# Kernel tuning notes

Measured on AMD Instinct MI355X. Metric: run time of the kernel, lower is better.

The kernel has to match this reference:

```python
import jax, jax.numpy as jnp
import numpy as np

M, A, H, T = 6, 4096, 128, 30   # num_modes, num_actors, hidden_size, future_steps
HIST = 50
MAX_T = 6.0
DT = MAX_T / T                   # min_stepsize: one Euler step per prediction interval
MIN_SCALE = 0.001
EPS = 1e-5

def _ln(x, g, b):
    mu = x.mean(-1, keepdims=True)
    v = ((x - mu) ** 2).mean(-1, keepdims=True)
    return (x - mu) * jax.lax.rsqrt(v + EPS) * g + b

def setup_inputs() -> dict:
    key = jax.random.key(0)
    ks = iter(jax.random.split(key, 64))
    def p(shape):
        return jax.random.normal(next(ks), shape, jnp.float32) * 0.02
    inp = {
        'local_embed':  jax.random.normal(next(ks), (A, H), jnp.float32),
        'global_embed': jax.random.normal(next(ks), (M, A, H), jnp.float32),
        'noise':        jax.random.normal(next(ks), (T, M * A, H), jnp.float32),
        # aggr_embed: Linear(2H,H) + LayerNorm
        'aggr_w': p((2 * H, H)), 'aggr_b': p((H,)),
        'aggr_g': jnp.ones((H,), jnp.float32), 'aggr_be': jnp.zeros((H,), jnp.float32),
        # FFunc (posterior drift): Linear(H+2,H)-Tanh-Linear(H,H)-Tanh-Linear(H,H)
        'f_w1': p((H + 2, H)), 'f_b1': p((H,)),
        'f_w2': p((H, H)),     'f_b2': p((H,)),
        'f_w3': p((H, H)),     'f_b3': p((H,)),
        # GFunc (diffusion): Linear(H+2,H)-Tanh-Linear(H,H)-Tanh-Linear(H,1)-Sigmoid
        'g_w1': p((H + 2, H)), 'g_b1': p((H,)),
        'g_w2': p((H, H)),     'g_b2': p((H,)),
        'g_w3': p((H, 1)),     'g_b3': p((1,)),
        # decoder: Linear(H,H)+LN+ReLU+Linear(H,2)
        'd_w1': p((H, H)), 'd_b1': p((H,)),
        'd_g': jnp.ones((H,), jnp.float32), 'd_be': jnp.zeros((H,), jnp.float32),
        'd_w2': p((H, 2)), 'd_b2': p((2,)),
        # scale head (uncertain=True): same structure as decoder
        's_w1': p((H, H)), 's_b1': p((H,)),
        's_g': jnp.ones((H,), jnp.float32), 's_be': jnp.zeros((H,), jnp.float32),
        's_w2': p((H, 2)), 's_b2': p((2,)),
        # pi head: Linear(2H,H)+LN+ReLU+Linear(H,1)
        'p_w1': p((2 * H, H)), 'p_b1': p((H,)),
        'p_g': jnp.ones((H,), jnp.float32), 'p_be': jnp.zeros((H,), jnp.float32),
        'p_w2': p((H, 1)), 'p_b2': p((1,)),
        'padding_mask': jnp.zeros((A, HIST), dtype=bool),
    }
    return inp

def reference(local_embed, global_embed, noise,
              aggr_w, aggr_b, aggr_g, aggr_be,
              f_w1, f_b1, f_w2, f_b2, f_w3, f_b3,
              g_w1, g_b1, g_w2, g_b2, g_w3, g_b3,
              d_w1, d_b1, d_g, d_be, d_w2, d_b2,
              s_w1, s_b1, s_g, s_be, s_w2, s_b2,
              p_w1, p_b1, p_g, p_be, p_w2, p_b2,
              padding_mask):
    N = M * A
    le = jnp.broadcast_to(local_embed, (M, A, H))
    # aggr_embed(cat(global, local))
    x = jnp.concatenate([global_embed, le], axis=-1)
    h0 = jax.nn.relu(_ln(x @ aggr_w + aggr_b, aggr_g, aggr_be)).reshape(N, H)

    def with_time(y, t):
        tc = jnp.ones((y.shape[0], 1), y.dtype) * t
        return jnp.concatenate([y, jnp.sin(tc), jnp.cos(tc)], axis=-1)

    def drift(t, y):  # FFunc
        i = with_time(y, t)
        h = jnp.tanh(i @ f_w1 + f_b1)
        h = jnp.tanh(h @ f_w2 + f_b2)
        return h @ f_w3 + f_b3

    def diffusion(t, y):  # GFunc -> scalar per sample, repeated over dims
        i = with_time(y, t)
        h = jnp.tanh(i @ g_w1 + g_b1)
        h = jnp.tanh(h @ g_w2 + g_b2)
        return jax.nn.sigmoid(h @ g_w3 + g_b3)  # [N,1]

    ts = jnp.linspace(0.0, MAX_T, T + 1)[:-1]  # left endpoints of each Euler step
    sqdt = jnp.sqrt(jnp.asarray(DT, h0.dtype))

    def step(y, tz):
        t, z = tz
        y2 = y + drift(t, y) * DT + diffusion(t, y) * sqdt * z
        return y2, y2

    _, ys = jax.lax.scan(step, h0, (ts, noise))  # [T, N, H]
    sol_y = ys.transpose(1, 0, 2)                # [N, T, H]

    dh = jax.nn.relu(_ln(sol_y @ d_w1 + d_b1, d_g, d_be))
    loc = (dh @ d_w2 + d_b2).reshape(M, A, T, 2)
    sh = jax.nn.relu(_ln(sol_y @ s_w1 + s_b1, s_g, s_be))
    scale = jax.nn.elu(sh @ s_w2 + s_b2) + 1.0 + MIN_SCALE
    scale = scale.reshape(M, A, T, 2)
    loc_out = jnp.concatenate([loc, scale], axis=-1)  # [M, A, T, 4]

    pin = jnp.concatenate([le, global_embed], axis=-1)
    pi = (jax.nn.relu(_ln(pin @ p_w1 + p_b1, p_g, p_be)) @ p_w2 + p_b2)
    pi = pi.squeeze(-1).T                              # [A, M]

    reg_mask = ~padding_mask[:, -T:]
    return loc_out, pi, reg_mask
```

## Files before the change

kernel.cpp:

```cpp
#include <hip/hip_runtime.h>

#define Adim 4096
#define HD 128
#define TSTEPS 30
#define NROWS 24576
#define RBLK 32
#define NBLKS 768
#define DT_C 0.2f
#define SQDT_C 0.44721359549995794f
#define LN_EPS 1e-5f

#define PI_OFF   2949120
#define MASK_OFF 2973696

typedef unsigned short u16;
typedef __bf16 bf16x8 __attribute__((ext_vector_type(8)));
typedef float f32x4 __attribute__((ext_vector_type(4)));

__device__ __forceinline__ u16 f2bf(float x){
    unsigned u = __builtin_bit_cast(unsigned, x);
    u = (u + 0x7fffu + ((u >> 16) & 1u)) >> 16;
    return (u16)u;
}
__device__ __forceinline__ float bf2f(unsigned h){
    unsigned u = (h & 0xffffu) << 16;
    return __builtin_bit_cast(float, u);
}
__device__ __forceinline__ unsigned pack2(float a, float b){
    unsigned r;
    asm("v_cvt_pk_bf16_f32 %0, %1, %2" : "=v"(r) : "v"(a), "v"(b));
    return r;
}
__device__ __forceinline__ float tanh_f(float x){
    return 1.0f - 2.0f / (1.0f + __expf(2.0f * x));
}
__device__ __forceinline__ float sigm_f(float x){
    return 1.0f / (1.0f + __expf(-x));
}
#define SWZ(r,k) ((k) ^ (((r)&7)<<3))

#define MFMA(A,B,C) __builtin_amdgcn_mfma_f32_16x16x32_bf16(A, B, C, 0, 0, 0)

__device__ __forceinline__ void loadW(const u16* __restrict__ img, int lane, int wid,
                                      bf16x8 W[4]) {
    const int c = wid*16 + (lane & 15);
    const int kq = lane >> 4;
#pragma unroll
    for (int kk = 0; kk < 4; ++kk)
        W[kk] = *reinterpret_cast<const bf16x8*>(img + c*HD + SWZ(c, kk*32 + kq*8));
}

__device__ __forceinline__ void gemm1(const u16* __restrict__ act, const bf16x8 (&W)[4],
                                      int lane, f32x4 acc[2]) {
    const int rl = lane & 15, kq = lane >> 4;
#pragma unroll
    for (int tr = 0; tr < 2; ++tr) {
        const int r = tr*16 + rl;
        const u16* arow = act + r*HD;
        f32x4 a = {0.f,0.f,0.f,0.f};
#pragma unroll
        for (int kk = 0; kk < 4; ++kk) {
            bf16x8 bf = *reinterpret_cast<const bf16x8*>(arow + SWZ(r, kk*32 + kq*8));
            a = MFMA(W[kk], bf, a);
        }
        acc[tr] = a;
    }
}
__device__ __forceinline__ void gemm2(const u16* __restrict__ act,
                                      const bf16x8 (&Wx)[4], const bf16x8 (&Wy)[4],
                                      int lane, f32x4 accX[2], f32x4 accY[2]) {
    const int rl = lane & 15, kq = lane >> 4;
#pragma unroll
    for (int tr = 0; tr < 2; ++tr) {
        const int r = tr*16 + rl;
        const u16* arow = act + r*HD;
        f32x4 ax = {0.f,0.f,0.f,0.f}, ay = {0.f,0.f,0.f,0.f};
#pragma unroll
        for (int kk = 0; kk < 4; ++kk) {
            bf16x8 bf = *reinterpret_cast<const bf16x8*>(arow + SWZ(r, kk*32 + kq*8));
            ax = MFMA(Wx[kk], bf, ax);
            ay = MFMA(Wy[kk], bf, ay);
        }
        accX[tr] = ax; accY[tr] = ay;
    }
}
__device__ __forceinline__ void gemm4(const u16* __restrict__ act,
                                      const bf16x8 (&W1)[4], const bf16x8 (&W2)[4],
                                      const bf16x8 (&W3)[4], const bf16x8 (&W4)[4],
                                      int lane, f32x4 a1[2], f32x4 a2[2],
                                      f32x4 a3[2], f32x4 a4[2]) {
    const int rl = lane & 15, kq = lane >> 4;
#pragma unroll
    for (int tr = 0; tr < 2; ++tr) {
        const int r = tr*16 + rl;
        const u16* arow = act + r*HD;
        f32x4 x1={0.f,0.f,0.f,0.f}, x2={0.f,0.f,0.f,0.f};
        f32x4 x3={0.f,0.f,0.f,0.f}, x4={0.f,0.f,0.f,0.f};
#pragma unroll
        for (int kk = 0; kk < 4; ++kk) {
            bf16x8 bf = *reinterpret_cast<const bf16x8*>(arow + SWZ(r, kk*32 + kq*8));
            x1 = MFMA(W1[kk], bf, x1);
            x2 = MFMA(W2[kk], bf, x2);
            x3 = MFMA(W3[kk], bf, x3);
            x4 = MFMA(W4[kk], bf, x4);
        }
        a1[tr]=x1; a2[tr]=x2; a3[tr]=x3; a4[tr]=x4;
    }
}

__device__ __forceinline__ void epiT(const f32x4 acc[2], const float b[4],
                                     u16* dst, int lane, int wid) {
    const int c0 = wid*16 + ((lane>>4)<<2);
    const int rl = lane & 15;
#pragma unroll
    for (int tr = 0; tr < 2; ++tr) {
        int r = tr*16 + rl;
        float v0 = tanh_f(acc[tr][0] + b[0]);
        float v1 = tanh_f(acc[tr][1] + b[1]);
        float v2 = tanh_f(acc[tr][2] + b[2]);
        float v3 = tanh_f(acc[tr][3] + b[3]);
        uint2 pk = { pack2(v0, v1), pack2(v2, v3) };
        *reinterpret_cast<uint2*>(dst + r*HD + SWZ(r, c0)) = pk;
    }
}
__device__ __forceinline__ void epiN(const f32x4 acc[2], const float b[4],
                                     u16* dst, int lane, int wid) {
    const int c0 = wid*16 + ((lane>>4)<<2);
    const int rl = lane & 15;
#pragma unroll
    for (int tr = 0; tr < 2; ++tr) {
        int r = tr*16 + rl;
        uint2 pk = { pack2(acc[tr][0]+b[0], acc[tr][1]+b[1]),
                     pack2(acc[tr][2]+b[2], acc[tr][3]+b[3]) };
        *reinterpret_cast<uint2*>(dst + r*HD + SWZ(r, c0)) = pk;
    }
}
__device__ __forceinline__ void epiF(const f32x4 acc[2], const float* __restrict__ bias,
                                     float* dst, int lane, int wid) {
    const int c0 = wid*16 + ((lane>>4)<<2);
    const int rl = lane & 15;
    float4 b4 = *reinterpret_cast<const float4*>(bias + c0);
#pragma unroll
    for (int tr = 0; tr < 2; ++tr) {
        int r = tr*16 + rl;
        float4 v = { acc[tr][0]+b4.x, acc[tr][1]+b4.y, acc[tr][2]+b4.z, acc[tr][3]+b4.w };
        *reinterpret_cast<float4*>(dst + r*HD + c0) = v;
    }
}

__device__ __forceinline__ void gemmX(const u16* __restrict__ Xc, int kBase,
                                      const u16* __restrict__ img,
                                      int lane, int wid, f32x4 acc[2], bool init) {
    bf16x8 W[4]; loadW(img, lane, wid, W);
    const int rl = lane & 15, kq = lane >> 4;
#pragma unroll
    for (int tr = 0; tr < 2; ++tr) {
        const int r = tr*16 + rl;
        const u16* arow = Xc + r*256;
        f32x4 a = init ? f32x4{0.f,0.f,0.f,0.f} : acc[tr];
#pragma unroll
        for (int kk = 0; kk < 4; ++kk) {
            bf16x8 bf = *reinterpret_cast<const bf16x8*>(arow + SWZ(r, kBase + kk*32 + kq*8));
            a = MFMA(W[kk], bf, a);
        }
        acc[tr] = a;
    }
}

__device__ __forceinline__ void head_ln(const u16* __restrict__ src,
                                        const float4* __restrict__ pp4,
                                        float b20, float b21, int elu, int off, int idx,
                                        float* __restrict__ outStage)
{
    int row = idx >> 3, sub = idx & 7;
    int c0 = sub * 16;
    uint4 p0 = *reinterpret_cast<const uint4*>(src + row*HD + SWZ(row, c0));
    uint4 p1 = *reinterpret_cast<const uint4*>(src + row*HD + SWZ(row, c0+8));
    float v[16];
    v[0]=bf2f(p0.x); v[1]=bf2f(p0.x>>16); v[2]=bf2f(p0.y); v[3]=bf2f(p0.y>>16);
    v[4]=bf2f(p0.z); v[5]=bf2f(p0.z>>16); v[6]=bf2f(p0.w); v[7]=bf2f(p0.w>>16);
    v[8]=bf2f(p1.x); v[9]=bf2f(p1.x>>16); v[10]=bf2f(p1.y); v[11]=bf2f(p1.y>>16);
    v[12]=bf2f(p1.z); v[13]=bf2f(p1.z>>16); v[14]=bf2f(p1.w); v[15]=bf2f(p1.w>>16);
    float s = 0.f, sq = 0.f;
#pragma unroll
    for (int i = 0; i < 16; ++i){ s += v[i]; sq += v[i]*v[i]; }
    s += __shfl_xor(s,1); sq += __shfl_xor(sq,1);
    s += __shfl_xor(s,2); sq += __shfl_xor(sq,2);
    s += __shfl_xor(s,4); sq += __shfl_xor(sq,4);
    float mu = s * (1.f/128.f);
    float rstd = rsqrtf(sq*(1.f/128.f) - mu*mu + LN_EPS);
    float a0 = 0.f, a1 = 0.f;
#pragma unroll
    for (int i = 0; i < 16; ++i){
        float4 p = pp4[(c0 + i) ^ sub];
        float h = (v[i]-mu)*rstd*p.x + p.y;
        h = fmaxf(h, 0.f);
        a0 += h * p.z; a1 += h * p.w;
    }
    a0 += __shfl_xor(a0,1); a1 += __shfl_xor(a1,1);
    a0 += __shfl_xor(a0,2); a1 += __shfl_xor(a1,2);
    a0 += __shfl_xor(a0,4); a1 += __shfl_xor(a1,4);
    if (sub == 0){
        a0 += b20; a1 += b21;
        if (elu){
            a0 = (a0 > 0.f ? a0 : __expf(a0)-1.f) + 1.001f;
            a1 = (a1 > 0.f ? a1 : __expf(a1)-1.f) + 1.001f;
        }
        outStage[row*4 + off]   = a0;
        outStage[row*4 + off+1] = a1;
    }
}

__global__ void prep_w(const float* __restrict__ fw1, const float* __restrict__ fw2,
                       const float* __restrict__ fw3, const float* __restrict__ gw1,
                       const float* __restrict__ gw2, const float* __restrict__ dw1,
                       const float* __restrict__ sw1, const float* __restrict__ aw,
                       const float* __restrict__ pw1, u16* __restrict__ ws)
{
    int img = blockIdx.y;
    int idx = blockIdx.x * 256 + threadIdx.x;
    int k = idx >> 7, j = idx & 127;
    const float* W = fw1; int sr = k;
    switch (img) {
        case 0: W = fw1; break;  case 1: W = fw2; break;  case 2: W = fw3; break;
        case 3: W = gw1; break;  case 4: W = gw2; break;
        case 5: W = dw1; break;  case 6: W = sw1; break;
        case 7: W = aw;  break;  case 8: W = aw;  sr = k + 128; break;
        case 9: W = pw1; break;  case 10: W = pw1; sr = k + 128; break;
    }
    ws[(size_t)img*16384 + j*128 + SWZ(j, k)] = f2bf(W[(size_t)sr*128 + j]);
}

__global__ void reorder_out(const float* __restrict__ wsOut, float* __restrict__ outp)
{
    __shared__ float tile[3840];
    int b = blockIdx.x;
    const float* src = wsOut + (size_t)b*3840;
#pragma unroll
    for (int j = 0; j < 15; ++j) {
        int idx = j*256 + threadIdx.x;
        int tt = idx >> 7, rc = idx & 127;
        int row = rc >> 2, c = idx & 3;
        tile[row*120 + tt*4 + c] = src[idx];
    }
    __syncthreads();
    float* dst = outp + (size_t)b*3840;
#pragma unroll
    for (int j = 0; j < 15; ++j) {
        int idx = j*256 + threadIdx.x;
        dst[idx] = tile[idx];
    }
}

__global__ __launch_bounds__(512, 2) void sde_fused(
    const float* __restrict__ lE, const float* __restrict__ gE,
    const float* __restrict__ noise,
    const float* __restrict__ aggr_b, const float* __restrict__ aggr_g, const float* __restrict__ aggr_be,
    const float* __restrict__ fw1, const float* __restrict__ fb1,
    const float* __restrict__ fb2, const float* __restrict__ fb3,
    const float* __restrict__ gw1, const float* __restrict__ gb1,
    const float* __restrict__ gb2, const float* __restrict__ gw3, const float* __restrict__ gb3,
    const float* __restrict__ db1, const float* __restrict__ dg, const float* __restrict__ dbe,
    const float* __restrict__ dw2, const float* __restrict__ db2,
    const float* __restrict__ sb1, const float* __restrict__ sg, const float* __restrict__ sbe,
    const float* __restrict__ sw2, const float* __restrict__ sb2,
    const float* __restrict__ pb1, const float* __restrict__ pg, const float* __restrict__ pbe,
    const float* __restrict__ pw2, const float* __restrict__ pb2,
    const unsigned char* __restrict__ pmask,
    const u16* __restrict__ wimg,
    float* __restrict__ wsOut,
    float* __restrict__ outp)
{
    __shared__ __align__(16) unsigned char SMEM[61952];
    u16*  Sb    = (u16*)SMEM;
    u16*  Ab    = (u16*)(SMEM + 8192);
    u16*  Bb    = (u16*)(SMEM + 16384);
    u16*  Cb    = (u16*)(SMEM + 24576);
    u16*  Fb    = (u16*)(SMEM + 32768);
    u16*  Db    = (u16*)(SMEM + 40960);
    u16*  Eb    = (u16*)(SMEM + 49152);
    float4* ppd = (float4*)(SMEM + 57344);
    float4* pps = (float4*)(SMEM + 59392);
    float* outStage = (float*)(SMEM + 61440);
    u16*  Xc    = (u16*)(SMEM + 40960);
    float* preLN = (float*)(SMEM + 8192);

    const int tid  = threadIdx.x;
    const int lane = tid & 63;
    const int wid  = tid >> 6;
    const int bid  = blockIdx.x;
    const int r0   = bid * RBLK;
    const int c0e  = wid*16 + ((lane>>4)<<2);

    if (tid < 128) {
        int cs = tid ^ ((tid >> 4) & 7);
        ppd[cs] = make_float4(dg[tid], dbe[tid], dw2[2*tid], dw2[2*tid+1]);
        pps[cs] = make_float4(sg[tid], sbe[tid], sw2[2*tid], sw2[2*tid+1]);
    }
#pragma unroll
    for (int i = 0; i < 2; ++i) {
        int gidx = i*512 + tid;
        int r = gidx >> 5;
        int k = (gidx & 31) * 8;
        int gr = r0 + r;
        const float* src = (k < HD) ? (gE + (size_t)gr*HD + k)
                                    : (lE + (size_t)(gr & (Adim-1))*HD + (k - HD));
        float4 v0 = reinterpret_cast<const float4*>(src)[0];
        float4 v1 = reinterpret_cast<const float4*>(src)[1];
        uint4 pk = { pack2(v0.x, v0.y), pack2(v0.z, v0.w),
                     pack2(v1.x, v1.y), pack2(v1.z, v1.w) };
        *reinterpret_cast<uint4*>(Xc + r*256 + SWZ(r, k)) = pk;
    }
    __syncthreads();

    f32x4 acc[2];

    gemmX(Xc, 0,   wimg + 10*16384, lane, wid, acc, true);
    gemmX(Xc, 128, wimg + 9*16384,  lane, wid, acc, false);
    epiF(acc, pb1, preLN, lane, wid);
    __syncthreads();
    {
        int row = tid >> 4, sub = tid & 15;
        int c0 = sub * 8;
        const float* yr = preLN + row*HD + c0;
        float v[8]; float s = 0.f, sq = 0.f;
#pragma unroll
        for (int i = 0; i < 8; ++i){ float x = yr[i]; v[i] = x; s += x; sq += x*x; }
        s += __shfl_xor(s,1); sq += __shfl_xor(sq,1);
        s += __shfl_xor(s,2); sq += __shfl_xor(sq,2);
        s += __shfl_xor(s,4); sq += __shfl_xor(sq,4);
        s += __shfl_xor(s,8); sq += __shfl_xor(sq,8);
        float mu = s*(1.f/128.f);
        float rstd = rsqrtf(sq*(1.f/128.f) - mu*mu + LN_EPS);
        float a0 = 0.f;
#pragma unroll
        for (int i = 0; i < 8; ++i){
            int cc = c0 + i;
            float h = (v[i]-mu)*rstd*pg[cc] + pbe[cc];
            a0 += fmaxf(h, 0.f) * pw2[cc];
        }
        a0 += __shfl_xor(a0,1); a0 += __shfl_xor(a0,2);
        a0 += __shfl_xor(a0,4); a0 += __shfl_xor(a0,8);
        if (sub == 0) {
            int gr = r0 + row;
            outp[PI_OFF + (size_t)(gr & (Adim-1))*6 + (gr >> 12)] = a0 + pb2[0];
        }
    }
    if (tid < RBLK) {
        int gr = r0 + tid;
        if (gr < Adim) {
            const unsigned char* pm = pmask + (size_t)gr*50 + 20;
            float* o = outp + MASK_OFF + (size_t)gr*TSTEPS;
#pragma unroll
            for (int i = 0; i < TSTEPS; ++i) o[i] = pm[i] ? 0.f : 1.f;
        }
    }
    __syncthreads();

    gemmX(Xc, 0,   wimg + 7*16384, lane, wid, acc, true);
    gemmX(Xc, 128, wimg + 8*16384, lane, wid, acc, false);
    __syncthreads();
    epiF(acc, aggr_b, preLN, lane, wid);
    __syncthreads();

    float y0,y1,y2,y3,y4,y5,y6,y7;
    {
        int row = tid >> 4, sub = tid & 15;
        int c0 = sub * 8;
        const float* yr = preLN + row*HD + c0;
        float v[8]; float s = 0.f, sq = 0.f;
#pragma unroll
        for (int i = 0; i < 8; ++i){ float x = yr[i]; v[i] = x; s += x; sq += x*x; }
        s += __shfl_xor(s,1); sq += __shfl_xor(sq,1);
        s += __shfl_xor(s,2); sq += __shfl_xor(sq,2);
        s += __shfl_xor(s,4); sq += __shfl_xor(sq,4);
        s += __shfl_xor(s,8); sq += __shfl_xor(sq,8);
        float mu = s*(1.f/128.f);
        float rstd = rsqrtf(sq*(1.f/128.f) - mu*mu + LN_EPS);
#pragma unroll
        for (int i = 0; i < 8; ++i){
            int cc = c0 + i;
            float h = (v[i]-mu)*rstd*aggr_g[cc] + aggr_be[cc];
            v[i] = fmaxf(h, 0.f);
        }
        y0=v[0]; y1=v[1]; y2=v[2]; y3=v[3]; y4=v[4]; y5=v[5]; y6=v[6]; y7=v[7];
        uint4 pk = { pack2(v[0],v[1]), pack2(v[2],v[3]),
                     pack2(v[4],v[5]), pack2(v[6],v[7]) };
        *reinterpret_cast<uint4*>(&Sb[row*HD + SWZ(row, c0)]) = pk;
    }

    bf16x8 WF1[4], WG1[4], WF2[4], WG2[4], WF3[4], WD1[4], WS1[4];
    loadW(wimg + 0*16384, lane, wid, WF1);
    loadW(wimg + 3*16384, lane, wid, WG1);
    loadW(wimg + 1*16384, lane, wid, WF2);
    loadW(wimg + 4*16384, lane, wid, WG2);
    loadW(wimg + 2*16384, lane, wid, WF3);
    loadW(wimg + 5*16384, lane, wid, WD1);
    loadW(wimg + 6*16384, lane, wid, WS1);

    float fb2c[4], gb2c[4], fb3c[4], db1c[4], sb1c[4];
    float fb1c[4], gb1c[4], fw1s[4], fw1cc[4], gw1s[4], gw1cc[4];
#pragma unroll
    for (int q = 0; q < 4; ++q) {
        int c = c0e + q;
        fb2c[q]=fb2[c]; gb2c[q]=gb2[c]; fb3c[q]=fb3[c]; db1c[q]=db1[c]; sb1c[q]=sb1[c];
        fb1c[q]=fb1[c]; gb1c[q]=gb1[c];
        fw1s[q]=fw1[128*HD+c]; fw1cc[q]=fw1[129*HD+c];
        gw1s[q]=gw1[128*HD+c]; gw1cc[q]=gw1[129*HD+c];
    }
    float g3r[8];
#pragma unroll
    for (int j = 0; j < 8; ++j) g3r[j] = gw3[(tid & 15)*8 + j];
    const float db20 = db2[0], db21 = db2[1];
    const float sb20 = sb2[0], sb21 = sb2[1];
    const float gb3v = gb3[0];

    float4 nz0, nz1;
    __syncthreads();

    {
        float bF[4], bG[4];
#pragma unroll
        for (int q = 0; q < 4; ++q) { bF[q] = fb1c[q] + fw1cc[q]; bG[q] = gb1c[q] + gw1cc[q]; }
        f32x4 aF[2], aG[2];
        gemm2(Sb, WF1, WG1, lane, aF, aG);
        epiT(aF, bF, Ab, lane, wid);
        epiT(aG, bG, Bb, lane, wid);
        const float* np = noise + ((size_t)r0)*HD + (size_t)tid*8;
        nz0 = reinterpret_cast<const float4*>(np)[0];
        nz1 = reinterpret_cast<const float4*>(np)[1];
    }
    __syncthreads();

    for (int k = 0; k < TSTEPS; ++k) {
        {
            f32x4 a1[2];
            gemm1(Ab, WF2, lane, a1);
            epiT(a1, fb2c, Cb, lane, wid);
            gemm1(Bb, WG2, lane, a1);
            epiT(a1, gb2c, Fb, lane, wid);
        }
        if (k) {
            if (tid < 256) head_ln(Db, ppd, db20, db21, 0, 0, tid, outStage);
            else           head_ln(Eb, pps, sb20, sb21, 1, 2, tid-256, outStage);
        }
        __syncthreads();
        {
            f32x4 a1[2];
            gemm1(Cb, WF3, lane, a1);
            epiN(a1, fb3c, Db, lane, wid);
        }
        float growv;
        {
            int row = tid >> 4, sub = tid & 15;
            uint4 pk = *reinterpret_cast<const uint4*>(Fb + row*HD + SWZ(row, sub*8));
            float s = bf2f(pk.x)*g3r[0] + bf2f(pk.x>>16)*g3r[1]
                    + bf2f(pk.y)*g3r[2] + bf2f(pk.y>>16)*g3r[3]
                    + bf2f(pk.z)*g3r[4] + bf2f(pk.z>>16)*g3r[5]
                    + bf2f(pk.w)*g3r[6] + bf2f(pk.w>>16)*g3r[7];
            s += __shfl_xor(s,1); s += __shfl_xor(s,2);
            s += __shfl_xor(s,4); s += __shfl_xor(s,8);
            growv = sigm_f(s + gb3v);
        }
        __syncthreads();
        {
            int row = tid >> 4, sub = tid & 15;
            int sk = SWZ(row, sub*8);
            uint4 dpk = *reinterpret_cast<const uint4*>(Db + row*HD + sk);
            float g = growv * SQDT_C;
            y0 += bf2f(dpk.x)     * DT_C + g*nz0.x;
            y1 += bf2f(dpk.x>>16) * DT_C + g*nz0.y;
            y2 += bf2f(dpk.y)     * DT_C + g*nz0.z;
            y3 += bf2f(dpk.y>>16) * DT_C + g*nz0.w;
            y4 += bf2f(dpk.z)     * DT_C + g*nz1.x;
            y5 += bf2f(dpk.z>>16) * DT_C + g*nz1.y;
            y6 += bf2f(dpk.w)     * DT_C + g*nz1.z;
            y7 += bf2f(dpk.w>>16) * DT_C + g*nz1.w;
            uint4 s4 = { pack2(y0,y1), pack2(y2,y3), pack2(y4,y5), pack2(y6,y7) };
            *reinterpret_cast<uint4*>(Sb + row*HD + sk) = s4;
        }
        __syncthreads();
        if (k < TSTEPS-1) {
            float t = (k+1) * DT_C;
            float st = __sinf(t), ct = __cosf(t);
            float bF[4], bG[4];
#pragma unroll
            for (int q = 0; q < 4; ++q) {
                bF[q] = fb1c[q] + st*fw1s[q] + ct*fw1cc[q];
                bG[q] = gb1c[q] + st*gw1s[q] + ct*gw1cc[q];
            }
            f32x4 aF[2], aG[2], aD[2], aS[2];
            gemm4(Sb, WF1, WG1, WD1, WS1, lane, aF, aG, aD, aS);
            epiT(aF, bF, Ab, lane, wid);
            epiT(aG, bG, Bb, lane, wid);
            epiN(aD, db1c, Db, lane, wid);
            epiN(aS, sb1c, Eb, lane, wid);
            const float* np = noise + ((size_t)(k+1)*NROWS + r0)*HD + (size_t)tid*8;
            nz0 = reinterpret_cast<const float4*>(np)[0];
            nz1 = reinterpret_cast<const float4*>(np)[1];
            if (k >= 1 && tid < 128)
                wsOut[((size_t)bid*TSTEPS + (k-1))*128 + tid] = outStage[tid];
        } else {
            f32x4 aD[2], aS[2];
            gemm2(Sb, WD1, WS1, lane, aD, aS);
            epiN(aD, db1c, Db, lane, wid);
            epiN(aS, sb1c, Eb, lane, wid);
            if (tid < 128)
                wsOut[((size_t)bid*TSTEPS + (TSTEPS-2))*128 + tid] = outStage[tid];
        }
        __syncthreads();
    }
    if (tid < 256) head_ln(Db, ppd, db20, db21, 0, 0, tid, outStage);
    else           head_ln(Eb, pps, sb20, sb21, 1, 2, tid-256, outStage);
    __syncthreads();
    if (tid < 128)
        wsOut[((size_t)bid*TSTEPS + (TSTEPS-1))*128 + tid] = outStage[tid];
}

extern "C" void kernel_launch(void* const* d_in, const int* in_sizes, int n_in,
                              void* d_out, int out_size, void* d_ws, size_t ws_size,
                              hipStream_t stream) {
    const float* lE      = (const float*)d_in[0];
    const float* gE      = (const float*)d_in[1];
    const float* noise   = (const float*)d_in[2];
    const float* aggr_w  = (const float*)d_in[3];
    const float* aggr_b  = (const float*)d_in[4];
    const float* aggr_g  = (const float*)d_in[5];
    const float* aggr_be = (const float*)d_in[6];
    const float* fw1 = (const float*)d_in[7];
    const float* fb1 = (const float*)d_in[8];
    const float* fw2 = (const float*)d_in[9];
    const float* fb2 = (const float*)d_in[10];
    const float* fw3 = (const float*)d_in[11];
    const float* fb3 = (const float*)d_in[12];
    const float* gw1 = (const float*)d_in[13];
    const float* gb1 = (const float*)d_in[14];
    const float* gw2 = (const float*)d_in[15];
    const float* gb2 = (const float*)d_in[16];
    const float* gw3 = (const float*)d_in[17];
    const float* gb3 = (const float*)d_in[18];
    const float* dw1 = (const float*)d_in[19];
    const float* db1 = (const float*)d_in[20];
    const float* dg  = (const float*)d_in[21];
    const float* dbe = (const float*)d_in[22];
    const float* dw2 = (const float*)d_in[23];
    const float* db2 = (const float*)d_in[24];
    const float* sw1 = (const float*)d_in[25];
    const float* sb1 = (const float*)d_in[26];
    const float* sg  = (const float*)d_in[27];
    const float* sbe = (const float*)d_in[28];
    const float* sw2 = (const float*)d_in[29];
    const float* sb2 = (const float*)d_in[30];
    const float* pw1 = (const float*)d_in[31];
    const float* pb1 = (const float*)d_in[32];
    const float* pg  = (const float*)d_in[33];
    const float* pbe = (const float*)d_in[34];
    const float* pw2 = (const float*)d_in[35];
    const float* pb2 = (const float*)d_in[36];
    const unsigned char* pmask = (const unsigned char*)d_in[37];
    float* outp = (float*)d_out;
    u16* wimg = (u16*)d_ws;
    float* wsOut = (float*)((char*)d_ws + 360448);

    prep_w<<<dim3(64, 11), 256, 0, stream>>>(fw1, fw2, fw3, gw1, gw2, dw1, sw1,
                                             aggr_w, pw1, wimg);
    sde_fused<<<NBLKS, 512, 0, stream>>>(
        lE, gE, noise, aggr_b, aggr_g, aggr_be,
        fw1, fb1, fb2, fb3,
        gw1, gb1, gb2, gw3, gb3,
        db1, dg, dbe, dw2, db2,
        sb1, sg, sbe, sw2, sb2,
        pb1, pg, pbe, pw2, pb2,
        pmask, wimg, wsOut, outp);
    reorder_out<<<NBLKS, 256, 0, stream>>>(wsOut, outp);
}
```

Baseline: 593.5 us.

## Stream MFMA weights per step and move biases to LDS to raise occupancy

Removes the seven register-resident bf16 weight fragments and the per-thread bias arrays. Each SDE step now reloads weight fragments from global memory just before each GEMM, and biases come from a new shared-memory table. The fused 4-way first-layer GEMM is split into two 2-way GEMMs, and launch bounds move from 2 to 4 blocks per SM to cut register pressure and raise occupancy. In exchange every step issues repeated weight loads from cache, and shared memory per block grows, which may still cap how many blocks fit per CU.

```diff
diff --git a/kernel.cpp b/kernel.cpp
--- a/kernel.cpp
+++ b/kernel.cpp
@@ -38,7 +38,6 @@
     return 1.0f / (1.0f + __expf(-x));
 }
 #define SWZ(r,k) ((k) ^ (((r)&7)<<3))
-
 #define MFMA(A,B,C) __builtin_amdgcn_mfma_f32_16x16x32_bf16(A, B, C, 0, 0, 0)
 
 __device__ __forceinline__ void loadW(const u16* __restrict__ img, int lane, int wid,
@@ -82,29 +81,6 @@
             ay = MFMA(Wy[kk], bf, ay);
         }
         accX[tr] = ax; accY[tr] = ay;
-    }
-}
-__device__ __forceinline__ void gemm4(const u16* __restrict__ act,
-                                      const bf16x8 (&W1)[4], const bf16x8 (&W2)[4],
-                                      const bf16x8 (&W3)[4], const bf16x8 (&W4)[4],
-                                      int lane, f32x4 a1[2], f32x4 a2[2],
-                                      f32x4 a3[2], f32x4 a4[2]) {
-    const int rl = lane & 15, kq = lane >> 4;
-#pragma unroll
-    for (int tr = 0; tr < 2; ++tr) {
-        const int r = tr*16 + rl;
-        const u16* arow = act + r*HD;
-        f32x4 x1={0.f,0.f,0.f,0.f}, x2={0.f,0.f,0.f,0.f};
-        f32x4 x3={0.f,0.f,0.f,0.f}, x4={0.f,0.f,0.f,0.f};
-#pragma unroll
-        for (int kk = 0; kk < 4; ++kk) {
-            bf16x8 bf = *reinterpret_cast<const bf16x8*>(arow + SWZ(r, kk*32 + kq*8));
-            x1 = MFMA(W1[kk], bf, x1);
-            x2 = MFMA(W2[kk], bf, x2);
-            x3 = MFMA(W3[kk], bf, x3);
-            x4 = MFMA(W4[kk], bf, x4);
-        }
-        a1[tr]=x1; a2[tr]=x2; a3[tr]=x3; a4[tr]=x4;
     }
 }
 
@@ -252,7 +228,7 @@
     }
 }
 
-__global__ __launch_bounds__(512, 2) void sde_fused(
+__global__ __launch_bounds__(512, 4) void sde_fused(
     const float* __restrict__ lE, const float* __restrict__ gE,
     const float* __restrict__ noise,
     const float* __restrict__ aggr_b, const float* __restrict__ aggr_g, const float* __restrict__ aggr_be,
@@ -271,7 +247,7 @@
     float* __restrict__ wsOut,
     float* __restrict__ outp)
 {
-    __shared__ __align__(16) unsigned char SMEM[61952];
+    __shared__ __align__(16) unsigned char SMEM[68096];
     u16*  Sb    = (u16*)SMEM;
     u16*  Ab    = (u16*)(SMEM + 8192);
     u16*  Bb    = (u16*)(SMEM + 16384);
@@ -279,9 +255,10 @@
     u16*  Fb    = (u16*)(SMEM + 32768);
     u16*  Db    = (u16*)(SMEM + 40960);
     u16*  Eb    = (u16*)(SMEM + 49152);
-    float4* ppd = (float4*)(SMEM + 57344);
-    float4* pps = (float4*)(SMEM + 59392);
-    float* outStage = (float*)(SMEM + 61440);
+    float* biasT = (float*)(SMEM + 57344);
+    float4* ppd = (float4*)(SMEM + 63488);
+    float4* pps = (float4*)(SMEM + 65536);
+    float* outStage = (float*)(SMEM + 67584);
     u16*  Xc    = (u16*)(SMEM + 40960);
     float* preLN = (float*)(SMEM + 8192);
 
@@ -296,6 +273,18 @@
         int cs = tid ^ ((tid >> 4) & 7);
         ppd[cs] = make_float4(dg[tid], dbe[tid], dw2[2*tid], dw2[2*tid+1]);
         pps[cs] = make_float4(sg[tid], sbe[tid], sw2[2*tid], sw2[2*tid+1]);
+        biasT[0*128+tid]  = fb1[tid];
+        biasT[1*128+tid]  = fw1[128*HD+tid];
+        biasT[2*128+tid]  = fw1[129*HD+tid];
+        biasT[3*128+tid]  = gb1[tid];
+        biasT[4*128+tid]  = gw1[128*HD+tid];
+        biasT[5*128+tid]  = gw1[129*HD+tid];
+        biasT[6*128+tid]  = fb2[tid];
+        biasT[7*128+tid]  = gb2[tid];
+        biasT[8*128+tid]  = fb3[tid];
+        biasT[9*128+tid]  = db1[tid];
+        biasT[10*128+tid] = sb1[tid];
+        biasT[11*128+tid] = gw3[tid];
     }
 #pragma unroll
     for (int i = 0; i < 2; ++i) {
@@ -389,28 +378,6 @@
         *reinterpret_cast<uint4*>(&Sb[row*HD + SWZ(row, c0)]) = pk;
     }
 
-    bf16x8 WF1[4], WG1[4], WF2[4], WG2[4], WF3[4], WD1[4], WS1[4];
-    loadW(wimg + 0*16384, lane, wid, WF1);
-    loadW(wimg + 3*16384, lane, wid, WG1);
-    loadW(wimg + 1*16384, lane, wid, WF2);
-    loadW(wimg + 4*16384, lane, wid, WG2);
-    loadW(wimg + 2*16384, lane, wid, WF3);
-    loadW(wimg + 5*16384, lane, wid, WD1);
-    loadW(wimg + 6*16384, lane, wid, WS1);
-
-    float fb2c[4], gb2c[4], fb3c[4], db1c[4], sb1c[4];
-    float fb1c[4], gb1c[4], fw1s[4], fw1cc[4], gw1s[4], gw1cc[4];
-#pragma unroll
-    for (int q = 0; q < 4; ++q) {
-        int c = c0e + q;
-        fb2c[q]=fb2[c]; gb2c[q]=gb2[c]; fb3c[q]=fb3[c]; db1c[q]=db1[c]; sb1c[q]=sb1[c];
-        fb1c[q]=fb1[c]; gb1c[q]=gb1[c];
-        fw1s[q]=fw1[128*HD+c]; fw1cc[q]=fw1[129*HD+c];
-        gw1s[q]=gw1[128*HD+c]; gw1cc[q]=gw1[129*HD+c];
-    }
-    float g3r[8];
-#pragma unroll
-    for (int j = 0; j < 8; ++j) g3r[j] = gw3[(tid & 15)*8 + j];
     const float db20 = db2[0], db21 = db2[1];
     const float sb20 = sb2[0], sb21 = sb2[1];
     const float gb3v = gb3[0];
@@ -420,10 +387,22 @@
 
     {
         float bF[4], bG[4];
-#pragma unroll
-        for (int q = 0; q < 4; ++q) { bF[q] = fb1c[q] + fw1cc[q]; bG[q] = gb1c[q] + gw1cc[q]; }
+        {
+            float4 b1 = *reinterpret_cast<const float4*>(biasT + 0*128 + c0e);
+            float4 cc = *reinterpret_cast<const float4*>(biasT + 2*128 + c0e);
+            float4 b2 = *reinterpret_cast<const float4*>(biasT + 3*128 + c0e);
+            float4 c2 = *reinterpret_cast<const float4*>(biasT + 5*128 + c0e);
+#pragma unroll
+            for (int q = 0; q < 4; ++q) {
+                bF[q] = ((const float*)&b1)[q] + ((const float*)&cc)[q];
+                bG[q] = ((const float*)&b2)[q] + ((const float*)&c2)[q];
+            }
+        }
+        bf16x8 W1[4], W2[4];
+        loadW(wimg + 0*16384, lane, wid, W1);
+        loadW(wimg + 3*16384, lane, wid, W2);
         f32x4 aF[2], aG[2];
-        gemm2(Sb, WF1, WG1, lane, aF, aG);
+        gemm2(Sb, W1, W2, lane, aF, aG);
         epiT(aF, bF, Ab, lane, wid);
         epiT(aG, bG, Bb, lane, wid);
         const float* np = noise + ((size_t)r0)*HD + (size_t)tid*8;
@@ -434,11 +413,19 @@
 
     for (int k = 0; k < TSTEPS; ++k) {
         {
+            float bF2[4], bG2[4];
+            float4 t6 = *reinterpret_cast<const float4*>(biasT + 6*128 + c0e);
+            float4 t7 = *reinterpret_cast<const float4*>(biasT + 7*128 + c0e);
+#pragma unroll
+            for (int q = 0; q < 4; ++q) { bF2[q]=((const float*)&t6)[q]; bG2[q]=((const float*)&t7)[q]; }
+            bf16x8 Wf[4];
+            loadW(wimg + 1*16384, lane, wid, Wf);
             f32x4 a1[2];
-            gemm1(Ab, WF2, lane, a1);
-            epiT(a1, fb2c, Cb, lane, wid);
-            gemm1(Bb, WG2, lane, a1);
-            epiT(a1, gb2c, Fb, lane, wid);
+            gemm1(Ab, Wf, lane, a1);
+            epiT(a1, bF2, Cb, lane, wid);
+            loadW(wimg + 4*16384, lane, wid, Wf);
+            gemm1(Bb, Wf, lane, a1);
+            epiT(a1, bG2, Fb, lane, wid);
         }
         if (k) {
             if (tid < 256) head_ln(Db, ppd, db20, db21, 0, 0, tid, outStage);
@@ -446,18 +433,26 @@
         }
         __syncthreads();
         {
+            float bF3[4];
+            float4 t8 = *reinterpret_cast<const float4*>(biasT + 8*128 + c0e);
+#pragma unroll
+            for (int q = 0; q < 4; ++q) bF3[q]=((const float*)&t8)[q];
+            bf16x8 Wf[4];
+            loadW(wimg + 2*16384, lane, wid, Wf);
             f32x4 a1[2];
-            gemm1(Cb, WF3, lane, a1);
-            epiN(a1, fb3c, Db, lane, wid);
+            gemm1(Cb, Wf, lane, a1);
+            epiN(a1, bF3, Db, lane, wid);
         }
         float growv;
         {
             int row = tid >> 4, sub = tid & 15;
+            float4 g0 = *reinterpret_cast<const float4*>(biasT + 11*128 + sub*8);
+            float4 g1 = *reinterpret_cast<const float4*>(biasT + 11*128 + sub*8 + 4);
             uint4 pk = *reinterpret_cast<const uint4*>(Fb + row*HD + SWZ(row, sub*8));
-            float s = bf2f(pk.x)*g3r[0] + bf2f(pk.x>>16)*g3r[1]
-                    + bf2f(pk.y)*g3r[2] + bf2f(pk.y>>16)*g3r[3]
-                    + bf2f(pk.z)*g3r[4] + bf2f(pk.z>>16)*g3r[5]
-                    + bf2f(pk.w)*g3r[6] + bf2f(pk.w>>16)*g3r[7];
+            float s = bf2f(pk.x)*g0.x + bf2f(pk.x>>16)*g0.y
+                    + bf2f(pk.y)*g0.z + bf2f(pk.y>>16)*g0.w
+                    + bf2f(pk.z)*g1.x + bf2f(pk.z>>16)*g1.y
+                    + bf2f(pk.w)*g1.z + bf2f(pk.w>>16)*g1.w;
             s += __shfl_xor(s,1); s += __shfl_xor(s,2);
             s += __shfl_xor(s,4); s += __shfl_xor(s,8);
             growv = sigm_f(s + gb3v);
@@ -483,28 +478,60 @@
         if (k < TSTEPS-1) {
             float t = (k+1) * DT_C;
             float st = __sinf(t), ct = __cosf(t);
-            float bF[4], bG[4];
-#pragma unroll
-            for (int q = 0; q < 4; ++q) {
-                bF[q] = fb1c[q] + st*fw1s[q] + ct*fw1cc[q];
-                bG[q] = gb1c[q] + st*gw1s[q] + ct*gw1cc[q];
+            float bF[4], bG[4], bD[4], bS[4];
+            {
+                float4 a0 = *reinterpret_cast<const float4*>(biasT + 0*128 + c0e);
+                float4 a1 = *reinterpret_cast<const float4*>(biasT + 1*128 + c0e);
+                float4 a2 = *reinterpret_cast<const float4*>(biasT + 2*128 + c0e);
+                float4 a3 = *reinterpret_cast<const float4*>(biasT + 3*128 + c0e);
+                float4 a4 = *reinterpret_cast<const float4*>(biasT + 4*128 + c0e);
+                float4 a5 = *reinterpret_cast<const float4*>(biasT + 5*128 + c0e);
+                float4 a9 = *reinterpret_cast<const float4*>(biasT + 9*128 + c0e);
+                float4 aa = *reinterpret_cast<const float4*>(biasT + 10*128 + c0e);
+#pragma unroll
+                for (int q = 0; q < 4; ++q) {
+                    bF[q] = ((const float*)&a0)[q] + st*((const float*)&a1)[q] + ct*((const float*)&a2)[q];
+                    bG[q] = ((const float*)&a3)[q] + st*((const float*)&a4)[q] + ct*((const float*)&a5)[q];
+                    bD[q] = ((const float*)&a9)[q];
+                    bS[q] = ((const float*)&aa)[q];
+                }
             }
-            f32x4 aF[2], aG[2], aD[2], aS[2];
-            gemm4(Sb, WF1, WG1, WD1, WS1, lane, aF, aG, aD, aS);
-            epiT(aF, bF, Ab, lane, wid);
-            epiT(aG, bG, Bb, lane, wid);
-            epiN(aD, db1c, Db, lane, wid);
-            epiN(aS, sb1c, Eb, lane, wid);
+            {
+                bf16x8 W1[4], W2[4];
+                loadW(wimg + 0*16384, lane, wid, W1);
+                loadW(wimg + 3*16384, lane, wid, W2);
+                f32x4 aF[2], aG[2];
+                gemm2(Sb, W1, W2, lane, aF, aG);
+                epiT(aF, bF, Ab, lane, wid);
+                epiT(aG, bG, Bb, lane, wid);
+            }
+            {
+                bf16x8 W1[4], W2[4];
+                loadW(wimg + 5*16384, lane, wid, W1);
+                loadW(wimg + 6*16384, lane, wid, W2);
+                f32x4 aD[2], aS2[2];
+                gemm2(Sb, W1, W2, lane, aD, aS2);
+                epiN(aD, bD, Db, lane, wid);
+                epiN(aS2, bS, Eb, lane, wid);
+            }
             const float* np = noise + ((size_t)(k+1)*NROWS + r0)*HD + (size_t)tid*8;
             nz0 = reinterpret_cast<const float4*>(np)[0];
             nz1 = reinterpret_cast<const float4*>(np)[1];
             if (k >= 1 && tid < 128)
                 wsOut[((size_t)bid*TSTEPS + (k-1))*128 + tid] = outStage[tid];
         } else {
-            f32x4 aD[2], aS[2];
-            gemm2(Sb, WD1, WS1, lane, aD, aS);
-            epiN(aD, db1c, Db, lane, wid);
-            epiN(aS, sb1c, Eb, lane, wid);
+            float bD[4], bS[4];
+            float4 a9 = *reinterpret_cast<const float4*>(biasT + 9*128 + c0e);
+            float4 aa = *reinterpret_cast<const float4*>(biasT + 10*128 + c0e);
+#pragma unroll
+            for (int q = 0; q < 4; ++q) { bD[q]=((const float*)&a9)[q]; bS[q]=((const float*)&aa)[q]; }
+            bf16x8 W1[4], W2[4];
+            loadW(wimg + 5*16384, lane, wid, W1);
+            loadW(wimg + 6*16384, lane, wid, W2);
+            f32x4 aD[2], aS2[2];
+            gemm2(Sb, W1, W2, lane, aD, aS2);
+            epiN(aD, bD, Db, lane, wid);
+            epiN(aS2, bS, Eb, lane, wid);
             if (tid < 128)
                 wsOut[((size_t)bid*TSTEPS + (TSTEPS-2))*128 + tid] = outStage[tid];
         }
```

New measurement: 1.071 ms. +80.5%, slower.
